# Kernel optimization log

Hardware: AMD Instinct MI355X
Metric: run time of the kernel (lower is better)

## Reference

```python
import jax, jax.numpy as jnp
import numpy as np


def setup_inputs() -> dict:
    key = jax.random.key(0)
    kq, kk, kv = jax.random.split(key, 3)
    B, H, N, D = 2, 16, 2048, 128
    q = jax.random.normal(kq, (B, H, N, D), dtype=jnp.float32)
    k = jax.random.normal(kk, (B, H, N, D), dtype=jnp.float32)
    v = jax.random.normal(kv, (B, H, N, D), dtype=jnp.float32)
    return {"q": q, "k": k, "v": v, "num_sink": 4, "window_size": 1024}


def reference(q, k, v, num_sink, window_size):
    # Sink + sliding-window causal attention (single-device path of the SP wrapper).
    # Query i attends to key j iff j <= i AND (j < num_sink OR i - j < window_size).
    B, H, N, D = q.shape
    scale = 1.0 / np.sqrt(D).astype(np.float32)
    i = jnp.arange(N)[:, None]   # query positions
    j = jnp.arange(N)[None, :]   # key positions
    mask = (j <= i) & ((j < num_sink) | ((i - j) < window_size))  # [N, N]
    scores = jnp.einsum('bhid,bhjd->bhij', q, k) * scale          # [B,H,N,N]
    scores = jnp.where(mask, scores, jnp.finfo(scores.dtype).min)
    attn = jax.nn.softmax(scores, axis=-1)
    return jnp.einsum('bhij,bhjd->bhid', attn, v)
```

## Files before the change

kernel.cpp:

```cpp
#include <hip/hip_runtime.h>
#include <stdint.h>

#define NN 2048
#define DD 128
#define BHH 32
#define QT 64
#define KT 64

typedef short v8s __attribute__((ext_vector_type(8)));
typedef short v4s __attribute__((ext_vector_type(4)));
typedef float v4f __attribute__((ext_vector_type(4)));
typedef float v16f __attribute__((ext_vector_type(16)));
typedef unsigned int u32;
typedef u32 u32x2 __attribute__((ext_vector_type(2)));
typedef u32 u32x4 __attribute__((ext_vector_type(4)));

__device__ __forceinline__ unsigned short f2bf(float x) {
  unsigned u = __builtin_bit_cast(unsigned, x);
  u += 0x7fffu + ((u >> 16) & 1u);
  return (unsigned short)(u >> 16);
}

__device__ __forceinline__ v8s cvt8(const float* __restrict__ p) {
  v8s r;
#pragma unroll
  for (int j = 0; j < 8; j++) r[j] = (short)f2bf(p[j]);
  return r;
}

__device__ __forceinline__ u32 pk2(float a, float b) {
  u32 r;
  asm("v_cvt_pk_bf16_f32 %0, %1, %2" : "=v"(r) : "v"(a), "v"(b));
  return r;
}

__global__ __launch_bounds__(256) void prep(const float* __restrict__ K, const float* __restrict__ V,
                     unsigned short* __restrict__ Kb, unsigned short* __restrict__ Vt) {
  const int z = blockIdx.z;
  const int tid = threadIdx.x;
  if (z >= BHH) {
    const int bh = z - BHH;
    const int chunk = blockIdx.y * 32 + blockIdx.x;
    size_t base = (size_t)bh * NN * DD + (size_t)chunk * 4096 + (size_t)tid * 16;
    v4f f0 = *(const v4f*)(K + base);
    v4f f1 = *(const v4f*)(K + base + 4);
    v4f f2 = *(const v4f*)(K + base + 8);
    v4f f3 = *(const v4f*)(K + base + 12);
    u32x4 w0 = { pk2(f0[0], f0[1]), pk2(f0[2], f0[3]), pk2(f1[0], f1[1]), pk2(f1[2], f1[3]) };
    u32x4 w1 = { pk2(f2[0], f2[1]), pk2(f2[2], f2[3]), pk2(f3[0], f3[1]), pk2(f3[2], f3[3]) };
    *(u32x4*)(Kb + base) = w0;
    *(u32x4*)(Kb + base + 8) = w1;
    return;
  }
  __shared__ __align__(16) unsigned short t[64 * 68];
  const int bh = z;
  const int n0b = blockIdx.x, d0b = blockIdx.y;
  const int c16 = tid & 15, r4 = tid >> 4;
  const float* src = V + ((size_t)bh * NN + n0b * 64 + r4 * 4) * DD + d0b * 64 + c16 * 4;
  v4f f0 = *(const v4f*)(src);
  v4f f1 = *(const v4f*)(src + DD);
  v4f f2 = *(const v4f*)(src + 2 * DD);
  v4f f3 = *(const v4f*)(src + 3 * DD);
#pragma unroll
  for (int j = 0; j < 4; j++) {
    u32x2 w = { pk2(f0[j], f1[j]), pk2(f2[j], f3[j]) };
    *(u32x2*)(t + (c16 * 4 + j) * 68 + r4 * 4) = w;
  }
  __syncthreads();
  unsigned short* Vfb = Vt + (size_t)bh * (512u * 512);
#pragma unroll
  for (int p = 0; p < 2; p++) {
    const int fid = p * 4 + (tid >> 6);
    const int ktl = fid >> 1, ncl = fid & 1;
    const int lane = tid & 63;
    const int dloc = ncl * 32 + (lane & 31);
    const int nloc = ktl * 16 + (lane >> 5) * 8;
    v4s x0 = *(const v4s*)(t + dloc * 68 + nloc);
    v4s x1 = *(const v4s*)(t + dloc * 68 + nloc + 4);
    v8s o = { x0[0], x0[1], x0[2], x0[3], x1[0], x1[1], x1[2], x1[3] };
    const size_t fi = (size_t)(n0b * 4 + ktl) * 4 + (d0b * 2 + ncl);
    *(v8s*)(Vfb + fi * 512 + (size_t)lane * 8) = o;
  }
}

template <bool PREPPED>
__global__ __launch_bounds__(256, 2) void attn(
    const float* __restrict__ Q,
    const float* __restrict__ Kf, const unsigned short* __restrict__ Kb,
    const unsigned short* __restrict__ Vfr, const float* __restrict__ Vf,
    const int* __restrict__ nsp, const int* __restrict__ wsp,
    float* __restrict__ O) {
  const int ns = nsp[0], win = wsp[0];
  const int x = blockIdx.x;
  const int xcd = x & 7, slot = x >> 3;
  const int bh = xcd + 8 * (slot / 24);
  const int jobid = slot % 24;
  int qis[2], njobs;
  if (jobid < 16) { njobs = 1; qis[0] = 31 - jobid; qis[1] = 0; }
  else { int p = jobid - 16; njobs = 2; qis[0] = 15 - p; qis[1] = p; }

  const int tid = threadIdx.x;
  const int wave = tid >> 6;
  const int team = wave >> 1;
  const int wv = wave & 1;
  const int l = tid & 63;
  const int m = l & 31;
  const int hi = l >> 5;
  const int rbase = 4 * hi;

  __shared__ __align__(16) unsigned short Kl[2][16 * 512];
  __shared__ float Ls[128];

  const float csc = 0.088388347648318447f * 1.4426950408889634f;

  const size_t kK = ((size_t)bh * NN + wv * 32 + m) * DD + hi * 8;
  const unsigned short* Vfb = Vfr + (size_t)bh * (512u * 512);

  auto mkpa = [&](float a0, float a1, float a2, float a3,
                  float b0, float b1, float b2, float b3) -> v8s {
    u32x2 r02 = __builtin_amdgcn_permlane32_swap(pk2(a0, a1), pk2(b0, b1), false, false);
    u32x2 r13 = __builtin_amdgcn_permlane32_swap(pk2(a2, a3), pk2(b2, b3), false, false);
    u32x4 pw = { r02[0], r13[0], r02[1], r13[1] };
    return __builtin_bit_cast(v8s, pw);
  };

  for (int ji = 0; ji < njobs; ji++) {
    const int q0 = qis[ji] * QT;
    const int qrow0w = q0 + wv * 32;
    const int qi = qrow0w + m;

    v8s qf[8];
    {
      const float* qb = Q + ((size_t)bh * NN + qi) * DD + hi * 8;
#pragma unroll
      for (int kc = 0; kc < 8; kc++) {
        v8s r;
#pragma unroll
        for (int e = 0; e < 8; e++) r[e] = (short)f2bf(qb[kc * 16 + e] * csc);
        qf[kc] = r;
      }
    }

    float lsum = 0.f;
    v16f oa[4];
#pragma unroll
    for (int nc = 0; nc < 4; nc++) oa[nc] = (v16f)(0.f);

    const int wstart = q0 - win + 1;
    const bool sink16 = (wstart > KT - 1) && (ns <= 16);
    const int kb_lo = sink16 ? ((wstart >> 6) << 6) : 0;
    const int kb_hi = q0 + QT;
    const int ntiles = (kb_hi - kb_lo) >> 6;
    const int T = (ntiles + 1) >> 1;

    v8s kst[8];
    auto stage_load = [&](int kb) {
#pragma unroll
      for (int i = 0; i < 8; i++) {
        if constexpr (PREPPED)
          kst[i] = *(const v8s*)(Kb + kK + (size_t)kb * DD + i * 16);
        else
          kst[i] = cvt8(Kf + kK + (size_t)kb * DD + i * 16);
      }
    };

    const int kb0 = kb_lo + team * KT;
    if (kb0 < kb_hi) stage_load(kb0);

    if (sink16 && team == 1) {
      v8s kf0[8];
      const size_t g0 = ((size_t)bh * NN + m) * DD + hi * 8;
#pragma unroll
      for (int kc = 0; kc < 8; kc++)
        kf0[kc] = PREPPED ? *(const v8s*)(Kb + g0 + kc * 16) : cvt8(Kf + g0 + kc * 16);
      v16f s = (v16f)(0.f);
#pragma unroll
      for (int kc = 0; kc < 8; kc++)
        s = __builtin_amdgcn_mfma_f32_32x32x16_bf16(kf0[kc], qf[kc], s, 0, 0, 0);
#pragma unroll
      for (int reg = 0; reg < 16; reg++) {
        const int kj = (reg & 3) + 8 * (reg >> 2) + rbase;
        const bool valid = (kj < ns) && (kj <= qi);
        s[reg] = valid ? __builtin_amdgcn_exp2f(s[reg]) : 0.f;
      }
      lsum += (((s[0] + s[1]) + (s[2] + s[3])) + ((s[4] + s[5]) + (s[6] + s[7])))
            + (((s[8] + s[9]) + (s[10] + s[11])) + ((s[12] + s[13]) + (s[14] + s[15])));
      v8s pa = mkpa(s[0], s[1], s[2], s[3], s[4], s[5], s[6], s[7]);
#pragma unroll
      for (int nc = 0; nc < 4; nc++) {
        v8s vf;
        if constexpr (PREPPED) {
          vf = *(const v8s*)(Vfb + (size_t)nc * 512 + (size_t)l * 8);
        } else {
#pragma unroll
          for (int e = 0; e < 8; e++)
            vf[e] = (short)f2bf(Vf[((size_t)bh * NN + hi * 8 + e) * DD + nc * 32 + m]);
        }
        oa[nc] = __builtin_amdgcn_mfma_f32_32x32x16_bf16(pa, vf, oa[nc], 0, 0, 0);
      }
    }

    for (int it = 0; it < T; ++it) {
      const int kb = kb_lo + (2 * it + team) * KT;
      const bool act = kb < kb_hi;
      __syncthreads();
      if (act) {
#pragma unroll
        for (int i = 0; i < 8; i++)
          *(v8s*)(Kl[team] + (wv * 8 + i) * 512 + l * 8) = kst[i];
      }
      __syncthreads();
      if (!act) continue;
      if (kb + 2 * KT < kb_hi) stage_load(kb + 2 * KT);

#pragma unroll
      for (int ct = 0; ct < 2; ct++) {
        v8s vf[8];
        if constexpr (PREPPED) {
#pragma unroll
          for (int i = 0; i < 8; i++) {
            const int ktl = i >> 2, nc = i & 3;
            vf[i] = *(const v8s*)(Vfb + ((size_t)((kb >> 4) + ct * 2 + ktl) * 4 + nc) * 512 + (size_t)l * 8);
          }
        } else {
#pragma unroll
          for (int i = 0; i < 8; i++) {
            const int ktl = i >> 2, nc = i & 3;
#pragma unroll
            for (int e = 0; e < 8; e++)
              vf[i][e] = (short)f2bf(Vf[((size_t)bh * NN + kb + (ct * 2 + ktl) * 16 + hi * 8 + e) * DD + nc * 32 + m]);
          }
        }

        v16f s = (v16f)(0.f);
        __builtin_amdgcn_s_setprio(1);
#pragma unroll
        for (int kc = 0; kc < 8; kc++) {
          v8s kfr = *(const v8s*)(Kl[team] + (ct * 8 + kc) * 512 + l * 8);
          s = __builtin_amdgcn_mfma_f32_32x32x16_bf16(kfr, qf[kc], s, 0, 0, 0);
        }
        __builtin_amdgcn_s_setprio(0);

        const int kbct = kb + ct * 32;
        const bool full = (kbct + 31 <= qrow0w) && (kbct >= qrow0w + 32 - win);
        if (full) {
#pragma unroll
          for (int reg = 0; reg < 16; reg++) s[reg] = __builtin_amdgcn_exp2f(s[reg]);
        } else {
#pragma unroll
          for (int reg = 0; reg < 16; reg++) {
            const int kj = kbct + (reg & 3) + 8 * (reg >> 2) + rbase;
            const bool valid = (kj <= qi) && ((kj < ns) || (qi - kj < win));
            s[reg] = valid ? __builtin_amdgcn_exp2f(s[reg]) : 0.f;
          }
        }
        lsum += (((s[0] + s[1]) + (s[2] + s[3])) + ((s[4] + s[5]) + (s[6] + s[7])))
              + (((s[8] + s[9]) + (s[10] + s[11])) + ((s[12] + s[13]) + (s[14] + s[15])));

        v8s pa0 = mkpa(s[0], s[1], s[2], s[3], s[4], s[5], s[6], s[7]);
        v8s pa1 = mkpa(s[8], s[9], s[10], s[11], s[12], s[13], s[14], s[15]);

        __builtin_amdgcn_s_setprio(1);
#pragma unroll
        for (int ktl = 0; ktl < 2; ktl++) {
          const v8s pf = ktl ? pa1 : pa0;
#pragma unroll
          for (int nc = 0; nc < 4; nc++)
            oa[nc] = __builtin_amdgcn_mfma_f32_32x32x16_bf16(pf, vf[ktl * 4 + nc], oa[nc], 0, 0, 0);
        }
        __builtin_amdgcn_s_setprio(0);
      }
    }

    __syncthreads();
    float* ex = (float*)&Kl[0][0];
    if (team == 1) {
#pragma unroll
      for (int nc = 0; nc < 4; nc++)
#pragma unroll
        for (int reg = 0; reg < 16; reg++)
          ex[(nc * 16 + reg) * 128 + wv * 64 + l] = oa[nc][reg];
      Ls[wv * 64 + l] = lsum;
    }
    __syncthreads();
    if (team == 0) {
#pragma unroll
      for (int nc = 0; nc < 4; nc++)
#pragma unroll
        for (int reg = 0; reg < 16; reg++)
          oa[nc][reg] += ex[(nc * 16 + reg) * 128 + wv * 64 + l];
      float lt = lsum + Ls[wv * 64 + l];
      lt += __shfl_xor(lt, 32, 64);
      const float inv = 1.f / lt;
      float* ob = O + ((size_t)bh * NN + qrow0w) * DD;
#pragma unroll
      for (int reg = 0; reg < 16; reg++) {
        const int row = (reg & 3) + 8 * (reg >> 2) + rbase;
        const float iv = __shfl(inv, row, 64);
#pragma unroll
        for (int nc = 0; nc < 4; nc++)
          ob[(size_t)row * DD + nc * 32 + m] = oa[nc][reg] * iv;
      }
    }
  }
}

extern "C" void kernel_launch(void* const* d_in, const int* in_sizes, int n_in,
                              void* d_out, int out_size, void* d_ws, size_t ws_size,
                              hipStream_t stream) {
  const float* q = (const float*)d_in[0];
  const float* k = (const float*)d_in[1];
  const float* v = (const float*)d_in[2];
  const int* nsp = (const int*)d_in[3];
  const int* wsp = (const int*)d_in[4];
  float* out = (float*)d_out;

  const size_t half = (size_t)BHH * NN * DD * sizeof(unsigned short);
  const int nblocks = BHH * 24;

  if (ws_size >= 2 * half) {
    unsigned short* kbf = (unsigned short*)d_ws;
    unsigned short* vfrag = (unsigned short*)((char*)d_ws + half);
    prep<<<dim3(32, 2, 2 * BHH), 256, 0, stream>>>(k, v, kbf, vfrag);
    attn<true><<<nblocks, 256, 0, stream>>>(q, k, kbf, vfrag, v, nsp, wsp, out);
  } else {
    attn<false><<<nblocks, 256, 0, stream>>>(q, k, nullptr, nullptr, v, nsp, wsp, out);
  }
}
```

Measured before the change: 209.0 us.

## Drop split-K wave teams; stream K fragments into LDS with direct global-to-LDS double buffer

The attention kernel goes from 4 waves (two teams splitting the key range, with an LDS reduction at the end) to 2 waves per block that each walk the whole key range. K is pre-laid out by prep in MFMA fragment order, so tiles can be loaded straight into a double-buffered LDS array via global_load_lds, which removes the register staging and LDS store step. The cross-team output/lsum reduction and its barriers go away, and the Q load is vectorized. In exchange there is half the wave-level parallelism per block, a longer serial loop per wave, and 16 V fragments held in registers per tile, which raises register pressure.

```diff
diff --git a/kernel.cpp b/kernel.cpp
--- a/kernel.cpp
+++ b/kernel.cpp
@@ -34,22 +34,28 @@
   return r;
 }
 
+__device__ __forceinline__ void gl_lds16(const unsigned short* g, unsigned short* l) {
+  __builtin_amdgcn_global_load_lds((const unsigned int*)g, (unsigned int*)l, 16, 0, 0);
+}
+
 __global__ __launch_bounds__(256) void prep(const float* __restrict__ K, const float* __restrict__ V,
                      unsigned short* __restrict__ Kb, unsigned short* __restrict__ Vt) {
   const int z = blockIdx.z;
   const int tid = threadIdx.x;
   if (z >= BHH) {
     const int bh = z - BHH;
-    const int chunk = blockIdx.y * 32 + blockIdx.x;
-    size_t base = (size_t)bh * NN * DD + (size_t)chunk * 4096 + (size_t)tid * 16;
-    v4f f0 = *(const v4f*)(K + base);
-    v4f f1 = *(const v4f*)(K + base + 4);
-    v4f f2 = *(const v4f*)(K + base + 8);
-    v4f f3 = *(const v4f*)(K + base + 12);
-    u32x4 w0 = { pk2(f0[0], f0[1]), pk2(f0[2], f0[3]), pk2(f1[0], f1[1]), pk2(f1[2], f1[3]) };
-    u32x4 w1 = { pk2(f2[0], f2[1]), pk2(f2[2], f2[3]), pk2(f3[0], f3[1]), pk2(f3[2], f3[3]) };
-    *(u32x4*)(Kb + base) = w0;
-    *(u32x4*)(Kb + base + 8) = w1;
+    const int kb32 = blockIdx.y * 32 + blockIdx.x;
+    const int m = tid & 31, kc = tid >> 5;
+    const float* src = K + ((size_t)bh * NN + kb32 * 32 + m) * DD + kc * 16;
+    v4f a0 = *(const v4f*)(src);
+    v4f a1 = *(const v4f*)(src + 4);
+    v4f a2 = *(const v4f*)(src + 8);
+    v4f a3 = *(const v4f*)(src + 12);
+    u32x4 w0 = { pk2(a0[0], a0[1]), pk2(a0[2], a0[3]), pk2(a1[0], a1[1]), pk2(a1[2], a1[3]) };
+    u32x4 w1 = { pk2(a2[0], a2[1]), pk2(a2[2], a2[3]), pk2(a3[0], a3[1]), pk2(a3[2], a3[3]) };
+    unsigned short* base = Kb + (((size_t)bh * 64 + kb32) * 8 + kc) * 512;
+    *(u32x4*)(base + (size_t)m * 8) = w0;
+    *(u32x4*)(base + (size_t)(32 + m) * 8) = w1;
     return;
   }
   __shared__ __align__(16) unsigned short t[64 * 68];
@@ -84,7 +90,8 @@
 }
 
 template <bool PREPPED>
-__global__ __launch_bounds__(256, 2) void attn(
+__global__ __launch_bounds__(128) __attribute__((amdgpu_waves_per_eu(1, 2)))
+void attn(
     const float* __restrict__ Q,
     const float* __restrict__ Kf, const unsigned short* __restrict__ Kb,
     const unsigned short* __restrict__ Vfr, const float* __restrict__ Vf,
@@ -100,20 +107,16 @@
   else { int p = jobid - 16; njobs = 2; qis[0] = 15 - p; qis[1] = p; }
 
   const int tid = threadIdx.x;
-  const int wave = tid >> 6;
-  const int team = wave >> 1;
-  const int wv = wave & 1;
+  const int w = tid >> 6;
   const int l = tid & 63;
   const int m = l & 31;
   const int hi = l >> 5;
   const int rbase = 4 * hi;
 
   __shared__ __align__(16) unsigned short Kl[2][16 * 512];
-  __shared__ float Ls[128];
 
   const float csc = 0.088388347648318447f * 1.4426950408889634f;
 
-  const size_t kK = ((size_t)bh * NN + wv * 32 + m) * DD + hi * 8;
   const unsigned short* Vfb = Vfr + (size_t)bh * (512u * 512);
 
   auto mkpa = [&](float a0, float a1, float a2, float a3,
@@ -126,7 +129,7 @@
 
   for (int ji = 0; ji < njobs; ji++) {
     const int q0 = qis[ji] * QT;
-    const int qrow0w = q0 + wv * 32;
+    const int qrow0w = q0 + w * 32;
     const int qi = qrow0w + m;
 
     v8s qf[8];
@@ -134,10 +137,11 @@
       const float* qb = Q + ((size_t)bh * NN + qi) * DD + hi * 8;
 #pragma unroll
       for (int kc = 0; kc < 8; kc++) {
-        v8s r;
-#pragma unroll
-        for (int e = 0; e < 8; e++) r[e] = (short)f2bf(qb[kc * 16 + e] * csc);
-        qf[kc] = r;
+        v4f a = *(const v4f*)(qb + kc * 16);
+        v4f b = *(const v4f*)(qb + kc * 16 + 4);
+        u32x4 pw = { pk2(a[0] * csc, a[1] * csc), pk2(a[2] * csc, a[3] * csc),
+                     pk2(b[0] * csc, b[1] * csc), pk2(b[2] * csc, b[3] * csc) };
+        qf[kc] = __builtin_bit_cast(v8s, pw);
       }
     }
 
@@ -150,157 +154,149 @@
     const bool sink16 = (wstart > KT - 1) && (ns <= 16);
     const int kb_lo = sink16 ? ((wstart >> 6) << 6) : 0;
     const int kb_hi = q0 + QT;
-    const int ntiles = (kb_hi - kb_lo) >> 6;
-    const int T = (ntiles + 1) >> 1;
-
-    v8s kst[8];
-    auto stage_load = [&](int kb) {
-#pragma unroll
-      for (int i = 0; i < 8; i++) {
-        if constexpr (PREPPED)
-          kst[i] = *(const v8s*)(Kb + kK + (size_t)kb * DD + i * 16);
-        else
-          kst[i] = cvt8(Kf + kK + (size_t)kb * DD + i * 16);
+
+    if constexpr (PREPPED) {
+      auto issueK = [&](int kb, int buf) {
+        const unsigned short* src =
+            Kb + (((size_t)bh * 64 + (kb >> 5) + w) * 8) * 512 + (size_t)l * 8;
+        unsigned short* dst = &Kl[buf][(w * 8) * 512];
+#pragma unroll
+        for (int i = 0; i < 8; i++)
+          gl_lds16(src + (size_t)i * 512, dst + i * 512);
+      };
+
+      int cur = 0;
+      issueK(kb_lo, 0);
+
+      if (sink16) {
+        v8s kf0[8];
+#pragma unroll
+        for (int kc = 0; kc < 8; kc++)
+          kf0[kc] = *(const v8s*)(Kb + ((size_t)bh * 64 * 8 + kc) * 512 + (size_t)l * 8);
+        v16f s = (v16f)(0.f);
+#pragma unroll
+        for (int kc = 0; kc < 8; kc++)
+          s = __builtin_amdgcn_mfma_f32_32x32x16_bf16(kf0[kc], qf[kc], s, 0, 0, 0);
+#pragma unroll
+        for (int reg = 0; reg < 16; reg++) {
+          const int kj = (reg & 3) + 8 * (reg >> 2) + rbase;
+          const bool valid = (kj < ns) && (kj <= qi);
+          s[reg] = valid ? __builtin_amdgcn_exp2f(s[reg]) : 0.f;
+        }
+        lsum += (((s[0] + s[1]) + (s[2] + s[3])) + ((s[4] + s[5]) + (s[6] + s[7])))
+              + (((s[8] + s[9]) + (s[10] + s[11])) + ((s[12] + s[13]) + (s[14] + s[15])));
+        v8s pa = mkpa(s[0], s[1], s[2], s[3], s[4], s[5], s[6], s[7]);
+#pragma unroll
+        for (int nc = 0; nc < 4; nc++) {
+          v8s vf = *(const v8s*)(Vfb + (size_t)nc * 512 + (size_t)l * 8);
+          oa[nc] = __builtin_amdgcn_mfma_f32_32x32x16_bf16(pa, vf, oa[nc], 0, 0, 0);
+        }
       }
-    };
-
-    const int kb0 = kb_lo + team * KT;
-    if (kb0 < kb_hi) stage_load(kb0);
-
-    if (sink16 && team == 1) {
-      v8s kf0[8];
-      const size_t g0 = ((size_t)bh * NN + m) * DD + hi * 8;
-#pragma unroll
-      for (int kc = 0; kc < 8; kc++)
-        kf0[kc] = PREPPED ? *(const v8s*)(Kb + g0 + kc * 16) : cvt8(Kf + g0 + kc * 16);
-      v16f s = (v16f)(0.f);
-#pragma unroll
-      for (int kc = 0; kc < 8; kc++)
-        s = __builtin_amdgcn_mfma_f32_32x32x16_bf16(kf0[kc], qf[kc], s, 0, 0, 0);
-#pragma unroll
-      for (int reg = 0; reg < 16; reg++) {
-        const int kj = (reg & 3) + 8 * (reg >> 2) + rbase;
-        const bool valid = (kj < ns) && (kj <= qi);
-        s[reg] = valid ? __builtin_amdgcn_exp2f(s[reg]) : 0.f;
+
+      asm volatile("s_waitcnt vmcnt(0)" ::: "memory");
+      __syncthreads();
+
+      for (int kb = kb_lo; kb < kb_hi; kb += KT) {
+        if (kb + KT < kb_hi) issueK(kb + KT, cur ^ 1);
+        v8s vf[16];
+#pragma unroll
+        for (int i = 0; i < 16; i++) {
+          const int kt = i >> 2, nc = i & 3;
+          vf[i] = *(const v8s*)(Vfb + ((size_t)((kb >> 4) + kt) * 4 + nc) * 512 + (size_t)l * 8);
+        }
+
+#pragma unroll
+        for (int ct = 0; ct < 2; ct++) {
+          v16f s = (v16f)(0.f);
+          __builtin_amdgcn_s_setprio(1);
+#pragma unroll
+          for (int kc = 0; kc < 8; kc++) {
+            v8s kfr = *(const v8s*)(&Kl[cur][(ct * 8 + kc) * 512 + l * 8]);
+            s = __builtin_amdgcn_mfma_f32_32x32x16_bf16(kfr, qf[kc], s, 0, 0, 0);
+          }
+          __builtin_amdgcn_s_setprio(0);
+
+          const int kbct = kb + ct * 32;
+          const bool full = (kbct + 31 <= qrow0w) && (kbct >= qrow0w + 32 - win);
+          if (full) {
+#pragma unroll
+            for (int reg = 0; reg < 16; reg++) s[reg] = __builtin_amdgcn_exp2f(s[reg]);
+          } else {
+#pragma unroll
+            for (int reg = 0; reg < 16; reg++) {
+              const int kj = kbct + (reg & 3) + 8 * (reg >> 2) + rbase;
+              const bool valid = (kj <= qi) && ((kj < ns) || (qi - kj < win));
+              s[reg] = valid ? __builtin_amdgcn_exp2f(s[reg]) : 0.f;
+            }
+          }
+          lsum += (((s[0] + s[1]) + (s[2] + s[3])) + ((s[4] + s[5]) + (s[6] + s[7])))
+                + (((s[8] + s[9]) + (s[10] + s[11])) + ((s[12] + s[13]) + (s[14] + s[15])));
+
+          v8s pa0 = mkpa(s[0], s[1], s[2], s[3], s[4], s[5], s[6], s[7]);
+          v8s pa1 = mkpa(s[8], s[9], s[10], s[11], s[12], s[13], s[14], s[15]);
+
+          __builtin_amdgcn_s_setprio(1);
+#pragma unroll
+          for (int ktl = 0; ktl < 2; ktl++) {
+            const v8s pf = ktl ? pa1 : pa0;
+#pragma unroll
+            for (int nc = 0; nc < 4; nc++)
+              oa[nc] = __builtin_amdgcn_mfma_f32_32x32x16_bf16(pf, vf[(ct * 2 + ktl) * 4 + nc],
+                                                               oa[nc], 0, 0, 0);
+          }
+          __builtin_amdgcn_s_setprio(0);
+        }
+
+        asm volatile("s_waitcnt vmcnt(0)" ::: "memory");
+        __syncthreads();
+        cur ^= 1;
       }
-      lsum += (((s[0] + s[1]) + (s[2] + s[3])) + ((s[4] + s[5]) + (s[6] + s[7])))
-            + (((s[8] + s[9]) + (s[10] + s[11])) + ((s[12] + s[13]) + (s[14] + s[15])));
-      v8s pa = mkpa(s[0], s[1], s[2], s[3], s[4], s[5], s[6], s[7]);
-#pragma unroll
-      for (int nc = 0; nc < 4; nc++) {
-        v8s vf;
-        if constexpr (PREPPED) {
-          vf = *(const v8s*)(Vfb + (size_t)nc * 512 + (size_t)l * 8);
-        } else {
-#pragma unroll
-          for (int e = 0; e < 8; e++)
-            vf[e] = (short)f2bf(Vf[((size_t)bh * NN + hi * 8 + e) * DD + nc * 32 + m]);
-        }
-        oa[nc] = __builtin_amdgcn_mfma_f32_32x32x16_bf16(pa, vf, oa[nc], 0, 0, 0);
+    } else {
+      for (int kb = 0; kb < kb_hi; kb += KT) {
+        if ((kb >= ns) && (kb + KT - 1 < wstart)) continue;
+#pragma unroll
+        for (int ct = 0; ct < 2; ct++) {
+          v16f s = (v16f)(0.f);
+#pragma unroll
+          for (int kc = 0; kc < 8; kc++) {
+            v8s kfr = cvt8(Kf + ((size_t)bh * NN + kb + ct * 32 + m) * DD + kc * 16 + hi * 8);
+            s = __builtin_amdgcn_mfma_f32_32x32x16_bf16(kfr, qf[kc], s, 0, 0, 0);
+          }
+#pragma unroll
+          for (int reg = 0; reg < 16; reg++) {
+            const int kj = kb + ct * 32 + (reg & 3) + 8 * (reg >> 2) + rbase;
+            const bool valid = (kj <= qi) && ((kj < ns) || (qi - kj < win));
+            s[reg] = valid ? __builtin_amdgcn_exp2f(s[reg]) : 0.f;
+            lsum += s[reg];
+          }
+          v8s pa0 = mkpa(s[0], s[1], s[2], s[3], s[4], s[5], s[6], s[7]);
+          v8s pa1 = mkpa(s[8], s[9], s[10], s[11], s[12], s[13], s[14], s[15]);
+#pragma unroll
+          for (int ktl = 0; ktl < 2; ktl++) {
+            const v8s pf = ktl ? pa1 : pa0;
+#pragma unroll
+            for (int nc = 0; nc < 4; nc++) {
+              v8s vfe;
+#pragma unroll
+              for (int e = 0; e < 8; e++)
+                vfe[e] = (short)f2bf(Vf[((size_t)bh * NN + kb + (ct * 2 + ktl) * 16 + hi * 8 + e) * DD + nc * 32 + m]);
+              oa[nc] = __builtin_amdgcn_mfma_f32_32x32x16_bf16(pf, vfe, oa[nc], 0, 0, 0);
+            }
+          }
+        }
       }
     }
 
-    for (int it = 0; it < T; ++it) {
-      const int kb = kb_lo + (2 * it + team) * KT;
-      const bool act = kb < kb_hi;
-      __syncthreads();
-      if (act) {
-#pragma unroll
-        for (int i = 0; i < 8; i++)
-          *(v8s*)(Kl[team] + (wv * 8 + i) * 512 + l * 8) = kst[i];
-      }
-      __syncthreads();
-      if (!act) continue;
-      if (kb + 2 * KT < kb_hi) stage_load(kb + 2 * KT);
-
-#pragma unroll
-      for (int ct = 0; ct < 2; ct++) {
-        v8s vf[8];
-        if constexpr (PREPPED) {
-#pragma unroll
-          for (int i = 0; i < 8; i++) {
-            const int ktl = i >> 2, nc = i & 3;
-            vf[i] = *(const v8s*)(Vfb + ((size_t)((kb >> 4) + ct * 2 + ktl) * 4 + nc) * 512 + (size_t)l * 8);
-          }
-        } else {
-#pragma unroll
-          for (int i = 0; i < 8; i++) {
-            const int ktl = i >> 2, nc = i & 3;
-#pragma unroll
-            for (int e = 0; e < 8; e++)
-              vf[i][e] = (short)f2bf(Vf[((size_t)bh * NN + kb + (ct * 2 + ktl) * 16 + hi * 8 + e) * DD + nc * 32 + m]);
-          }
-        }
-
-        v16f s = (v16f)(0.f);
-        __builtin_amdgcn_s_setprio(1);
-#pragma unroll
-        for (int kc = 0; kc < 8; kc++) {
-          v8s kfr = *(const v8s*)(Kl[team] + (ct * 8 + kc) * 512 + l * 8);
-          s = __builtin_amdgcn_mfma_f32_32x32x16_bf16(kfr, qf[kc], s, 0, 0, 0);
-        }
-        __builtin_amdgcn_s_setprio(0);
-
-        const int kbct = kb + ct * 32;
-        const bool full = (kbct + 31 <= qrow0w) && (kbct >= qrow0w + 32 - win);
-        if (full) {
-#pragma unroll
-          for (int reg = 0; reg < 16; reg++) s[reg] = __builtin_amdgcn_exp2f(s[reg]);
-        } else {
-#pragma unroll
-          for (int reg = 0; reg < 16; reg++) {
-            const int kj = kbct + (reg & 3) + 8 * (reg >> 2) + rbase;
-            const bool valid = (kj <= qi) && ((kj < ns) || (qi - kj < win));
-            s[reg] = valid ? __builtin_amdgcn_exp2f(s[reg]) : 0.f;
-          }
-        }
-        lsum += (((s[0] + s[1]) + (s[2] + s[3])) + ((s[4] + s[5]) + (s[6] + s[7])))
-              + (((s[8] + s[9]) + (s[10] + s[11])) + ((s[12] + s[13]) + (s[14] + s[15])));
-
-        v8s pa0 = mkpa(s[0], s[1], s[2], s[3], s[4], s[5], s[6], s[7]);
-        v8s pa1 = mkpa(s[8], s[9], s[10], s[11], s[12], s[13], s[14], s[15]);
-
-        __builtin_amdgcn_s_setprio(1);
-#pragma unroll
-        for (int ktl = 0; ktl < 2; ktl++) {
-          const v8s pf = ktl ? pa1 : pa0;
-#pragma unroll
-          for (int nc = 0; nc < 4; nc++)
-            oa[nc] = __builtin_amdgcn_mfma_f32_32x32x16_bf16(pf, vf[ktl * 4 + nc], oa[nc], 0, 0, 0);
-        }
-        __builtin_amdgcn_s_setprio(0);
-      }
-    }
-
-    __syncthreads();
-    float* ex = (float*)&Kl[0][0];
-    if (team == 1) {
+    float lt = lsum + __shfl_xor(lsum, 32, 64);
+    const float inv = 1.f / lt;
+    float* ob = O + ((size_t)bh * NN + qrow0w) * DD;
+#pragma unroll
+    for (int reg = 0; reg < 16; reg++) {
+      const int row = (reg & 3) + 8 * (reg >> 2) + rbase;
+      const float iv = __shfl(inv, row, 64);
 #pragma unroll
       for (int nc = 0; nc < 4; nc++)
-#pragma unroll
-        for (int reg = 0; reg < 16; reg++)
-          ex[(nc * 16 + reg) * 128 + wv * 64 + l] = oa[nc][reg];
-      Ls[wv * 64 + l] = lsum;
-    }
-    __syncthreads();
-    if (team == 0) {
-#pragma unroll
-      for (int nc = 0; nc < 4; nc++)
-#pragma unroll
-        for (int reg = 0; reg < 16; reg++)
-          oa[nc][reg] += ex[(nc * 16 + reg) * 128 + wv * 64 + l];
-      float lt = lsum + Ls[wv * 64 + l];
-      lt += __shfl_xor(lt, 32, 64);
-      const float inv = 1.f / lt;
-      float* ob = O + ((size_t)bh * NN + qrow0w) * DD;
-#pragma unroll
-      for (int reg = 0; reg < 16; reg++) {
-        const int row = (reg & 3) + 8 * (reg >> 2) + rbase;
-        const float iv = __shfl(inv, row, 64);
-#pragma unroll
-        for (int nc = 0; nc < 4; nc++)
-          ob[(size_t)row * DD + nc * 32 + m] = oa[nc][reg] * iv;
-      }
+        ob[(size_t)row * DD + nc * 32 + m] = oa[nc][reg] * iv;
     }
   }
 }
@@ -319,11 +315,11 @@
   const int nblocks = BHH * 24;
 
   if (ws_size >= 2 * half) {
-    unsigned short* kbf = (unsigned short*)d_ws;
+    unsigned short* kfrag = (unsigned short*)d_ws;
     unsigned short* vfrag = (unsigned short*)((char*)d_ws + half);
-    prep<<<dim3(32, 2, 2 * BHH), 256, 0, stream>>>(k, v, kbf, vfrag);
-    attn<true><<<nblocks, 256, 0, stream>>>(q, k, kbf, vfrag, v, nsp, wsp, out);
+    prep<<<dim3(32, 2, 2 * BHH), 256, 0, stream>>>(k, v, kfrag, vfrag);
+    attn<true><<<nblocks, 128, 0, stream>>>(q, k, kfrag, vfrag, v, nsp, wsp, out);
   } else {
-    attn<false><<<nblocks, 256, 0, stream>>>(q, k, nullptr, nullptr, v, nsp, wsp, out);
-  }
-}
+    attn<false><<<nblocks, 128, 0, stream>>>(q, k, nullptr, nullptr, v, nsp, wsp, out);
+  }
+}
```

After: 191.0 us. -8.6%, faster.
